# Performance work log

Hardware: AMD Instinct MI355X
Metric: run time of the kernel (lower is better)

Reference implementation:

```python
import jax, jax.numpy as jnp
import numpy as np

V, E, EH, H = 32000, 512, 1024, 512  # vocab, emb_dim, enc_hidden, dec_hidden
B, S = 16, 128


def setup_inputs() -> dict:
    key = jax.random.key(0)
    ks = jax.random.split(key, 8)
    g = lambda k, shape, scale: (jax.random.normal(k, shape, jnp.float32) * scale)
    return {
        "y": jax.random.randint(ks[0], (B, S), 0, V),
        "hn": jax.random.normal(ks[1], (B, 1, EH), jnp.float32),
        "emb": g(ks[2], (V, E), 0.02),          # embedding table
        "W_ih": g(ks[3], (3 * H, E), 0.05),      # GRU input weights (r,z,n)
        "W_hh": g(ks[4], (3 * H, H), 0.05),      # GRU hidden weights (r,z,n)
        "b_ih": jnp.zeros((3 * H,), jnp.float32),
        "b_hh": jnp.zeros((3 * H,), jnp.float32),
        "fc_w": g(ks[5], (H, EH), 0.03),         # fc: enc_hidden -> dec_hidden
        "fc_b": jnp.zeros((H,), jnp.float32),
        "pred_w": g(ks[6], (V, H), 0.03),        # pred: dec_hidden -> vocab
        "pred_b": jnp.zeros((V,), jnp.float32),
    }


def gru_scan(x, h0, W_ih, W_hh, b_ih, b_hh):
    """Single-layer unidirectional GRU (PyTorch gate order r,z,n).
    x: [B,S,E], h0: [B,H] -> outputs [B,S,H]."""
    h_dim = h0.shape[-1]
    # precompute input projections for all timesteps: [B,S,3H]
    gx = jnp.einsum('bse,ge->bsg', x, W_ih) + b_ih
    Wr, Wz, Wn = W_hh[:h_dim], W_hh[h_dim:2 * h_dim], W_hh[2 * h_dim:]
    br, bz, bn = b_hh[:h_dim], b_hh[h_dim:2 * h_dim], b_hh[2 * h_dim:]

    def step(h, g):
        gr, gz, gn = g[:, :h_dim], g[:, h_dim:2 * h_dim], g[:, 2 * h_dim:]
        r = jax.nn.sigmoid(gr + h @ Wr.T + br)
        z = jax.nn.sigmoid(gz + h @ Wz.T + bz)
        n = jnp.tanh(gn + r * (h @ Wn.T + bn))
        h_new = (1.0 - z) * n + z * h
        return h_new, h_new

    _, outs = jax.lax.scan(step, h0, jnp.swapaxes(gx, 0, 1))  # [S,B,H]
    return jnp.swapaxes(outs, 0, 1)  # [B,S,H]


def reference(y, hn, emb, W_ih, W_hh, b_ih, b_hh, fc_w, fc_b, pred_w, pred_b):
    # hn: [B,1,EH] -> fc -> [B,1,H] -> permute(1,0,2) -> initial hidden [B,H]
    h0 = (hn @ fc_w.T + fc_b)[:, 0, :]
    x = emb[y]  # [B,S,E]; dropout is identity in eval mode
    out = gru_scan(x, h0, W_ih, W_hh, b_ih, b_hh)  # [B,S,H]
    return out @ pred_w.T + pred_b  # [B,S,V]
```

## Files before the change

### kernel.cpp

```cpp
#include <hip/hip_runtime.h>


typedef __attribute__((ext_vector_type(8))) short           bf8_t;
typedef __attribute__((ext_vector_type(8))) unsigned short  us8_t;
typedef __attribute__((ext_vector_type(4))) unsigned short  us4_t;
typedef __attribute__((ext_vector_type(4))) float           f4_t;
typedef __attribute__((ext_vector_type(4))) unsigned int    u4_t;

#define SENT 0xFFFFFFFFu

__device__ __forceinline__ unsigned short f2bf(float x) {
    unsigned u = __builtin_bit_cast(unsigned, x);
    u += 0x7FFFu + ((u >> 16) & 1u);
    return (unsigned short)(u >> 16);
}
__device__ __forceinline__ float sigm(float x) { return 1.0f / (1.0f + __expf(-x)); }

__device__ __forceinline__ bf8_t mk_frag(f4_t v0, f4_t v1) {
    bf8_t f;
    f[0] = (short)f2bf(v0[0]); f[1] = (short)f2bf(v0[1]);
    f[2] = (short)f2bf(v0[2]); f[3] = (short)f2bf(v0[3]);
    f[4] = (short)f2bf(v1[0]); f[5] = (short)f2bf(v1[1]);
    f[6] = (short)f2bf(v1[2]); f[7] = (short)f2bf(v1[3]);
    return f;
}

__device__ __forceinline__ void llc_store_u32(unsigned int* p, unsigned int v) {
    asm volatile("global_store_dword %0, %1, off sc0 sc1" :: "v"(p), "v"(v) : "memory");
}

__global__ void k_fill(unsigned int* __restrict__ p) {
    int i = blockIdx.x * blockDim.x + threadIdx.x;
    u4_t v = {SENT, SENT, SENT, SENT};
    ((u4_t*)p)[i] = v;
}

__global__ void k_conv(const float* __restrict__ src, unsigned short* __restrict__ dst, int n4) {
    int i = blockIdx.x * blockDim.x + threadIdx.x;
    int stride = gridDim.x * blockDim.x;
    for (; i < n4; i += stride) {
        f4_t v = ((const f4_t*)src)[i];
        us4_t o;
        o[0] = f2bf(v[0]); o[1] = f2bf(v[1]); o[2] = f2bf(v[2]); o[3] = f2bf(v[3]);
        ((us4_t*)dst)[i] = o;
    }
}

__global__ void k_gather(const int* __restrict__ y, const float* __restrict__ emb,
                         unsigned short* __restrict__ xbf) {
    int m = blockIdx.x;
    int row = y[m];
    int t = threadIdx.x;
    f4_t v = ((const f4_t*)(emb + (size_t)row * 512))[t];
    us4_t o;
    o[0] = f2bf(v[0]); o[1] = f2bf(v[1]); o[2] = f2bf(v[2]); o[3] = f2bf(v[3]);
    ((us4_t*)(xbf + (size_t)m * 512))[t] = o;
}

__global__ void k_h0(const float* __restrict__ hn, const float* __restrict__ fc_w,
                     const float* __restrict__ fc_b, float* __restrict__ h0m) {
    __shared__ float sh[1024];
    int b = blockIdx.x, t = threadIdx.x;
    for (int i = t; i < 1024; i += 256) sh[i] = hn[b * 1024 + i];
    __syncthreads();
    int j = t;
    float a0 = fc_b[j], a1 = fc_b[j + 256];
    const float* w0 = fc_w + (size_t)j * 1024;
    const float* w1 = fc_w + (size_t)(j + 256) * 1024;
    #pragma unroll 8
    for (int e = 0; e < 1024; e++) { float he = sh[e]; a0 += he * w0[e]; a1 += he * w1[e]; }
    h0m[b * 512 + j] = a0;
    h0m[b * 512 + j + 256] = a1;
}

__launch_bounds__(256)
__global__ void k_gemm(const unsigned short* __restrict__ A, const unsigned short* __restrict__ Bt,
                       const float* __restrict__ bias, float* __restrict__ C, int N) {
    __shared__ unsigned short sA[128 * 64];
    __shared__ unsigned short sB[128 * 64];
    const int m0 = blockIdx.y * 128, n0 = blockIdx.x * 128;
    const int tid = threadIdx.x, lane = tid & 63, wave = tid >> 6;
    const int wm = wave >> 1, wn = wave & 1;
    f4_t acc[4][4] = {};
    for (int ks = 0; ks < 8; ks++) {
        const int k0 = ks * 64;
        #pragma unroll
        for (int t = 0; t < 4; t++) {
            int idx = tid + t * 256;
            int row = idx >> 3, slot = idx & 7;
            int sw = ((slot ^ (row & 7)) << 3);
            *(us8_t*)(&sA[row * 64 + sw]) = *(const us8_t*)(A + (size_t)(m0 + row) * 512 + k0 + slot * 8);
            *(us8_t*)(&sB[row * 64 + sw]) = *(const us8_t*)(Bt + (size_t)(n0 + row) * 512 + k0 + slot * 8);
        }
        __syncthreads();
        #pragma unroll
        for (int kk = 0; kk < 2; kk++) {
            bf8_t af[4], bfr[4];
            #pragma unroll
            for (int mi = 0; mi < 4; mi++) {
                int row = wm * 64 + mi * 16 + (lane & 15);
                int slot = (kk * 4 + (lane >> 4)) ^ (row & 7);
                af[mi] = *(const bf8_t*)(&sA[row * 64 + slot * 8]);
            }
            #pragma unroll
            for (int ni = 0; ni < 4; ni++) {
                int row = wn * 64 + ni * 16 + (lane & 15);
                int slot = (kk * 4 + (lane >> 4)) ^ (row & 7);
                bfr[ni] = *(const bf8_t*)(&sB[row * 64 + slot * 8]);
            }
            #pragma unroll
            for (int mi = 0; mi < 4; mi++)
                #pragma unroll
                for (int ni = 0; ni < 4; ni++)
                    acc[mi][ni] = __builtin_amdgcn_mfma_f32_16x16x32_bf16(af[mi], bfr[ni], acc[mi][ni], 0, 0, 0);
        }
        __syncthreads();
    }
    #pragma unroll
    for (int ni = 0; ni < 4; ni++) {
        int col = n0 + wn * 64 + ni * 16 + (lane & 15);
        float bv = bias[col];
        #pragma unroll
        for (int mi = 0; mi < 4; mi++) {
            int rbase = m0 + wm * 64 + mi * 16 + (lane >> 4) * 4;
            #pragma unroll
            for (int r = 0; r < 4; r++)
                C[(size_t)(rbase + r) * N + col] = acc[mi][ni][r] + bv;
        }
    }
}

__launch_bounds__(128, 1)
__global__ void k_rec(const float* __restrict__ W_hh, const float* __restrict__ b_hh,
                      const float* __restrict__ gx, const float* __restrict__ h0m,
                      unsigned int* __restrict__ hbuf, unsigned short* __restrict__ Hout) {
    const int c = blockIdx.x;
    const int tid = threadIdx.x;
    const int lane = tid & 63;
    const int w = tid >> 6;
    const int col = c * 16 + (lane & 15);
    const int kgrp = lane >> 4;
    const int bbase = kgrp * 4;

    __shared__ float sPart[2][12][64];

    bf8_t wfR[8], wfZ[8], wfN[8];
    {
        const f4_t* wr = (const f4_t*)(W_hh + (size_t)col * 512);
        const f4_t* wz = (const f4_t*)(W_hh + (size_t)(512 + col) * 512);
        const f4_t* wn = (const f4_t*)(W_hh + (size_t)(1024 + col) * 512);
        const int fo = kgrp * 2;
        #pragma unroll
        for (int j = 0; j < 8; j++) {
            const int kk = w * 8 + j;
            wfR[j] = mk_frag(wr[kk * 8 + fo], wr[kk * 8 + fo + 1]);
            wfZ[j] = mk_frag(wz[kk * 8 + fo], wz[kk * 8 + fo + 1]);
            wfN[j] = mk_frag(wn[kk * 8 + fo], wn[kk * 8 + fo + 1]);
        }
    }

    float brv = 0.f, bzv = 0.f, bnv = 0.f;
    f4_t h_reg = {0.f, 0.f, 0.f, 0.f};
    if (w == 0) {
        brv = b_hh[col]; bzv = b_hh[512 + col]; bnv = b_hh[1024 + col];
        #pragma unroll
        for (int r = 0; r < 4; r++) h_reg[r] = h0m[(bbase + r) * 512 + col];
        #pragma unroll
        for (int r = 0; r < 4; r++) {
            unsigned int hb = f2bf(h_reg[r]);
            unsigned int pr = __shfl_xor(hb, 1, 64);
            if (!(lane & 1))
                llc_store_u32(&hbuf[(bbase + r) * 256 + (col >> 1)], hb | (pr << 16));
        }
    }

    for (int s = 1; s <= 128; s++) {
        float gxr[4], gxz[4], gxn[4];
        if (w == 0) {
            #pragma unroll
            for (int r = 0; r < 4; r++) {
                const float* gp = gx + (size_t)((bbase + r) * 128 + (s - 1)) * 1536 + col;
                gxr[r] = gp[0]; gxz[r] = gp[512]; gxn[r] = gp[1024];
            }
        }

        const unsigned int* base = hbuf + (size_t)(s - 1) * 4096
                                 + (lane & 15) * 256 + kgrp * 4 + w * 128;
        u4_t q[8];
        int spins = 0;
        bool ok;
        do {
            asm volatile(
                "global_load_dwordx4 %0, %8, off sc0 sc1\n\t"
                "global_load_dwordx4 %1, %8, off offset:64 sc0 sc1\n\t"
                "global_load_dwordx4 %2, %8, off offset:128 sc0 sc1\n\t"
                "global_load_dwordx4 %3, %8, off offset:192 sc0 sc1\n\t"
                "global_load_dwordx4 %4, %8, off offset:256 sc0 sc1\n\t"
                "global_load_dwordx4 %5, %8, off offset:320 sc0 sc1\n\t"
                "global_load_dwordx4 %6, %8, off offset:384 sc0 sc1\n\t"
                "global_load_dwordx4 %7, %8, off offset:448 sc0 sc1\n\t"
                "s_waitcnt vmcnt(0)"
                : "=&v"(q[0]), "=&v"(q[1]), "=&v"(q[2]), "=&v"(q[3]),
                  "=&v"(q[4]), "=&v"(q[5]), "=&v"(q[6]), "=&v"(q[7])
                : "v"(base)
                : "memory");
            ok = true;
            #pragma unroll
            for (int j = 0; j < 8; j++)
                #pragma unroll
                for (int i = 0; i < 4; i++)
                    ok = ok && (q[j][i] != SENT);
        } while (!__all(ok) && ++spins < (1 << 20));
        __builtin_amdgcn_sched_barrier(0);

        f4_t aR = {}, aZ = {}, aN = {};
        #pragma unroll
        for (int j = 0; j < 8; j++) {
            bf8_t af = __builtin_bit_cast(bf8_t, q[j]);
            aR = __builtin_amdgcn_mfma_f32_16x16x32_bf16(af, wfR[j], aR, 0, 0, 0);
            aZ = __builtin_amdgcn_mfma_f32_16x16x32_bf16(af, wfZ[j], aZ, 0, 0, 0);
            aN = __builtin_amdgcn_mfma_f32_16x16x32_bf16(af, wfN[j], aN, 0, 0, 0);
        }

        const int slot = s & 1;
        if (w == 1) {
            #pragma unroll
            for (int r = 0; r < 4; r++) {
                sPart[slot][r][lane]     = aR[r];
                sPart[slot][4 + r][lane] = aZ[r];
                sPart[slot][8 + r][lane] = aN[r];
            }
        }
        __syncthreads();
        if (w == 0) {
            #pragma unroll
            for (int r = 0; r < 4; r++) {
                const int b = bbase + r;
                float pR = aR[r] + sPart[slot][r][lane];
                float pZ = aZ[r] + sPart[slot][4 + r][lane];
                float pN = aN[r] + sPart[slot][8 + r][lane];
                float rr = sigm(gxr[r] + pR + brv);
                float zz = sigm(gxz[r] + pZ + bzv);
                float nn = tanhf(gxn[r] + rr * (pN + bnv));
                float hnew = (1.f - zz) * nn + zz * h_reg[r];
                h_reg[r] = hnew;
                unsigned int hb = f2bf(hnew);
                Hout[(size_t)(b * 128 + (s - 1)) * 512 + col] = (unsigned short)hb;
                unsigned int pr = __shfl_xor(hb, 1, 64);
                if (!(lane & 1))
                    llc_store_u32(&hbuf[(size_t)s * 4096 + b * 256 + (col >> 1)], hb | (pr << 16));
            }
        }
    }
}

extern "C" void kernel_launch(void* const* d_in, const int* in_sizes, int n_in,
                              void* d_out, int out_size, void* d_ws, size_t ws_size,
                              hipStream_t stream) {
    const int*   y      = (const int*)  d_in[0];
    const float* hn     = (const float*)d_in[1];
    const float* emb    = (const float*)d_in[2];
    const float* W_ih   = (const float*)d_in[3];
    const float* W_hh   = (const float*)d_in[4];
    const float* b_ih   = (const float*)d_in[5];
    const float* b_hh   = (const float*)d_in[6];
    const float* fc_w   = (const float*)d_in[7];
    const float* fc_b   = (const float*)d_in[8];
    const float* pred_w = (const float*)d_in[9];
    const float* pred_b = (const float*)d_in[10];
    float* out = (float*)d_out;

    char* ws = (char*)d_ws;
    size_t off = 0;
    auto alloc = [&](size_t bytes) { void* p = ws + off; off = (off + bytes + 255) & ~(size_t)255; return p; };
    unsigned int*   hbuf   = (unsigned int*)   alloc((size_t)129 * 4096 * 4);
    float*          h0m    = (float*)          alloc((size_t)16 * 512 * 4);
    float*          gx     = (float*)          alloc((size_t)2048 * 1536 * 4);
    unsigned short* Hout   = (unsigned short*) alloc((size_t)2048 * 512 * 2);
    unsigned short* xbf    = (unsigned short*) alloc((size_t)2048 * 512 * 2);
    unsigned short* wihbf  = (unsigned short*) alloc((size_t)1536 * 512 * 2);
    unsigned short* pwbf   = (unsigned short*) alloc((size_t)32000 * 512 * 2);
    (void)ws_size; (void)in_sizes; (void)n_in; (void)out_size;

    k_fill  <<<516,  256, 0, stream>>>(hbuf);
    k_conv  <<<4096, 256, 0, stream>>>(pred_w, pwbf, 32000 * 512 / 4);
    k_conv  <<<512,  256, 0, stream>>>(W_ih,  wihbf, 1536 * 512 / 4);
    k_gather<<<2048, 128, 0, stream>>>(y, emb, xbf);
    k_h0    <<<16,   256, 0, stream>>>(hn, fc_w, fc_b, h0m);
    dim3 gG(12, 16);
    k_gemm  <<<gG, 256, 0, stream>>>(xbf, wihbf, b_ih, gx, 1536);
    k_rec   <<<32, 128, 0, stream>>>(W_hh, b_hh, gx, h0m, hbuf, Hout);
    dim3 gP(250, 16);
    k_gemm  <<<gP, 256, 0, stream>>>(Hout, pwbf, pred_b, out, 32000);
}
```

Before: 692.4 us.

## Fuse GRU recurrence with vocab projection GEMM via persistent tile queue

Merges the recurrent kernel and the output projection GEMM into one persistent kernel of 256 blocks. Sixteen blocks run the GRU scan with 32 columns each, and the remaining blocks pull output tiles from an atomic ticket. Each tile waits on sentinel-marked hidden states, so the projection overlaps with later timesteps. Hidden states are stored in timestep-major order and the output index is permuted back. Sigmoid and tanh are replaced with rcp/exp approximations. The change risks spinning blocks competing for resources and lower accuracy in the activations.

Result: faster. 645.0 us (-6.8%).

```diff
diff --git a/kernel.cpp b/kernel.cpp
--- a/kernel.cpp
+++ b/kernel.cpp
@@ -14,7 +14,13 @@
     u += 0x7FFFu + ((u >> 16) & 1u);
     return (unsigned short)(u >> 16);
 }
-__device__ __forceinline__ float sigm(float x) { return 1.0f / (1.0f + __expf(-x)); }
+__device__ __forceinline__ float fsigm(float x) {
+    return __builtin_amdgcn_rcpf(1.f + __expf(-x));
+}
+__device__ __forceinline__ float ftanh(float x) {
+    float e = __expf(2.f * x);
+    return 1.f - 2.f * __builtin_amdgcn_rcpf(e + 1.f);
+}
 
 __device__ __forceinline__ bf8_t mk_frag(f4_t v0, f4_t v1) {
     bf8_t f;
@@ -29,10 +35,13 @@
     asm volatile("global_store_dword %0, %1, off sc0 sc1" :: "v"(p), "v"(v) : "memory");
 }
 
-__global__ void k_fill(unsigned int* __restrict__ p) {
+__global__ void k_fill(unsigned int* __restrict__ hbuf, unsigned int* __restrict__ hout,
+                       int* __restrict__ ticket) {
+    if (blockIdx.x == 0 && threadIdx.x == 0) *ticket = 0;
     int i = blockIdx.x * blockDim.x + threadIdx.x;
     u4_t v = {SENT, SENT, SENT, SENT};
-    ((u4_t*)p)[i] = v;
+    if (i < 132096) ((u4_t*)hbuf)[i] = v;
+    else            ((u4_t*)hout)[i - 132096] = v;
 }
 
 __global__ void k_conv(const float* __restrict__ src, unsigned short* __restrict__ dst, int n4) {
@@ -130,125 +139,252 @@
     }
 }
 
-__launch_bounds__(128, 1)
-__global__ void k_rec(const float* __restrict__ W_hh, const float* __restrict__ b_hh,
-                      const float* __restrict__ gx, const float* __restrict__ h0m,
-                      unsigned int* __restrict__ hbuf, unsigned short* __restrict__ Hout) {
-    const int c = blockIdx.x;
+__launch_bounds__(256, 1)
+__global__ void k_fused(const float* __restrict__ W_hh, const float* __restrict__ b_hh,
+                        const float* __restrict__ gx, const float* __restrict__ h0m,
+                        unsigned int* __restrict__ hbuf, unsigned int* __restrict__ HoutP,
+                        const unsigned short* __restrict__ pwbf, const float* __restrict__ pred_b,
+                        float* __restrict__ out, int* __restrict__ tticket) {
+    __shared__ __align__(16) unsigned char smem[32768];
+    __shared__ int s_tile;
     const int tid = threadIdx.x;
     const int lane = tid & 63;
-    const int w = tid >> 6;
-    const int col = c * 16 + (lane & 15);
-    const int kgrp = lane >> 4;
-    const int bbase = kgrp * 4;
-
-    __shared__ float sPart[2][12][64];
-
-    bf8_t wfR[8], wfZ[8], wfN[8];
-    {
-        const f4_t* wr = (const f4_t*)(W_hh + (size_t)col * 512);
-        const f4_t* wz = (const f4_t*)(W_hh + (size_t)(512 + col) * 512);
-        const f4_t* wn = (const f4_t*)(W_hh + (size_t)(1024 + col) * 512);
-        const int fo = kgrp * 2;
-        #pragma unroll
-        for (int j = 0; j < 8; j++) {
-            const int kk = w * 8 + j;
-            wfR[j] = mk_frag(wr[kk * 8 + fo], wr[kk * 8 + fo + 1]);
-            wfZ[j] = mk_frag(wz[kk * 8 + fo], wz[kk * 8 + fo + 1]);
-            wfN[j] = mk_frag(wn[kk * 8 + fo], wn[kk * 8 + fo + 1]);
-        }
-    }
-
-    float brv = 0.f, bzv = 0.f, bnv = 0.f;
-    f4_t h_reg = {0.f, 0.f, 0.f, 0.f};
-    if (w == 0) {
-        brv = b_hh[col]; bzv = b_hh[512 + col]; bnv = b_hh[1024 + col];
-        #pragma unroll
-        for (int r = 0; r < 4; r++) h_reg[r] = h0m[(bbase + r) * 512 + col];
-        #pragma unroll
-        for (int r = 0; r < 4; r++) {
-            unsigned int hb = f2bf(h_reg[r]);
-            unsigned int pr = __shfl_xor(hb, 1, 64);
-            if (!(lane & 1))
-                llc_store_u32(&hbuf[(bbase + r) * 256 + (col >> 1)], hb | (pr << 16));
-        }
-    }
-
-    for (int s = 1; s <= 128; s++) {
-        float gxr[4], gxz[4], gxn[4];
+    const int wave = tid >> 6;
+
+    if (blockIdx.x < 16) {
+        float* sPart = (float*)smem;
+        const int c = blockIdx.x;
+        const int ch = wave >> 1, w = wave & 1;
+        const int col = c * 32 + ch * 16 + (lane & 15);
+        const int kgrp = lane >> 4, bbase = kgrp * 4;
+
+        bf8_t wfR[8], wfZ[8], wfN[8];
+        {
+            const f4_t* wr = (const f4_t*)(W_hh + (size_t)col * 512);
+            const f4_t* wz = (const f4_t*)(W_hh + (size_t)(512 + col) * 512);
+            const f4_t* wn = (const f4_t*)(W_hh + (size_t)(1024 + col) * 512);
+            const int fo = kgrp * 2;
+            #pragma unroll
+            for (int j = 0; j < 8; j++) {
+                const int kk = w * 8 + j;
+                wfR[j] = mk_frag(wr[kk * 8 + fo], wr[kk * 8 + fo + 1]);
+                wfZ[j] = mk_frag(wz[kk * 8 + fo], wz[kk * 8 + fo + 1]);
+                wfN[j] = mk_frag(wn[kk * 8 + fo], wn[kk * 8 + fo + 1]);
+            }
+        }
+        float brv = 0.f, bzv = 0.f, bnv = 0.f;
+        f4_t h_reg = {0.f, 0.f, 0.f, 0.f};
         if (w == 0) {
+            brv = b_hh[col]; bzv = b_hh[512 + col]; bnv = b_hh[1024 + col];
+            #pragma unroll
+            for (int r = 0; r < 4; r++) h_reg[r] = h0m[(bbase + r) * 512 + col];
             #pragma unroll
             for (int r = 0; r < 4; r++) {
-                const float* gp = gx + (size_t)((bbase + r) * 128 + (s - 1)) * 1536 + col;
-                gxr[r] = gp[0]; gxz[r] = gp[512]; gxn[r] = gp[1024];
-            }
-        }
-
-        const unsigned int* base = hbuf + (size_t)(s - 1) * 4096
-                                 + (lane & 15) * 256 + kgrp * 4 + w * 128;
-        u4_t q[8];
-        int spins = 0;
-        bool ok;
-        do {
-            asm volatile(
-                "global_load_dwordx4 %0, %8, off sc0 sc1\n\t"
-                "global_load_dwordx4 %1, %8, off offset:64 sc0 sc1\n\t"
-                "global_load_dwordx4 %2, %8, off offset:128 sc0 sc1\n\t"
-                "global_load_dwordx4 %3, %8, off offset:192 sc0 sc1\n\t"
-                "global_load_dwordx4 %4, %8, off offset:256 sc0 sc1\n\t"
-                "global_load_dwordx4 %5, %8, off offset:320 sc0 sc1\n\t"
-                "global_load_dwordx4 %6, %8, off offset:384 sc0 sc1\n\t"
-                "global_load_dwordx4 %7, %8, off offset:448 sc0 sc1\n\t"
-                "s_waitcnt vmcnt(0)"
-                : "=&v"(q[0]), "=&v"(q[1]), "=&v"(q[2]), "=&v"(q[3]),
-                  "=&v"(q[4]), "=&v"(q[5]), "=&v"(q[6]), "=&v"(q[7])
-                : "v"(base)
-                : "memory");
-            ok = true;
-            #pragma unroll
-            for (int j = 0; j < 8; j++)
-                #pragma unroll
-                for (int i = 0; i < 4; i++)
-                    ok = ok && (q[j][i] != SENT);
-        } while (!__all(ok) && ++spins < (1 << 20));
-        __builtin_amdgcn_sched_barrier(0);
-
-        f4_t aR = {}, aZ = {}, aN = {};
-        #pragma unroll
-        for (int j = 0; j < 8; j++) {
-            bf8_t af = __builtin_bit_cast(bf8_t, q[j]);
-            aR = __builtin_amdgcn_mfma_f32_16x16x32_bf16(af, wfR[j], aR, 0, 0, 0);
-            aZ = __builtin_amdgcn_mfma_f32_16x16x32_bf16(af, wfZ[j], aZ, 0, 0, 0);
-            aN = __builtin_amdgcn_mfma_f32_16x16x32_bf16(af, wfN[j], aN, 0, 0, 0);
-        }
-
-        const int slot = s & 1;
-        if (w == 1) {
-            #pragma unroll
-            for (int r = 0; r < 4; r++) {
-                sPart[slot][r][lane]     = aR[r];
-                sPart[slot][4 + r][lane] = aZ[r];
-                sPart[slot][8 + r][lane] = aN[r];
-            }
-        }
-        __syncthreads();
-        if (w == 0) {
-            #pragma unroll
-            for (int r = 0; r < 4; r++) {
-                const int b = bbase + r;
-                float pR = aR[r] + sPart[slot][r][lane];
-                float pZ = aZ[r] + sPart[slot][4 + r][lane];
-                float pN = aN[r] + sPart[slot][8 + r][lane];
-                float rr = sigm(gxr[r] + pR + brv);
-                float zz = sigm(gxz[r] + pZ + bzv);
-                float nn = tanhf(gxn[r] + rr * (pN + bnv));
-                float hnew = (1.f - zz) * nn + zz * h_reg[r];
-                h_reg[r] = hnew;
-                unsigned int hb = f2bf(hnew);
-                Hout[(size_t)(b * 128 + (s - 1)) * 512 + col] = (unsigned short)hb;
+                unsigned int hb = f2bf(h_reg[r]);
                 unsigned int pr = __shfl_xor(hb, 1, 64);
                 if (!(lane & 1))
-                    llc_store_u32(&hbuf[(size_t)s * 4096 + b * 256 + (col >> 1)], hb | (pr << 16));
+                    llc_store_u32(&hbuf[(bbase + r) * 256 + (col >> 1)], hb | (pr << 16));
+            }
+        }
+
+        for (int s = 1; s <= 128; s++) {
+            float gxr[4], gxz[4], gxn[4];
+            if (w == 0) {
+                #pragma unroll
+                for (int r = 0; r < 4; r++) {
+                    const float* gp = gx + (size_t)((bbase + r) * 128 + (s - 1)) * 1536 + col;
+                    gxr[r] = gp[0]; gxz[r] = gp[512]; gxn[r] = gp[1024];
+                }
+            }
+            const unsigned int* base = hbuf + (size_t)(s - 1) * 4096
+                                     + (lane & 15) * 256 + kgrp * 4 + w * 128;
+            u4_t q[8];
+            int spins = 0;
+            bool ok;
+            do {
+                asm volatile(
+                    "global_load_dwordx4 %0, %8, off sc0 sc1\n\t"
+                    "global_load_dwordx4 %1, %8, off offset:64 sc0 sc1\n\t"
+                    "global_load_dwordx4 %2, %8, off offset:128 sc0 sc1\n\t"
+                    "global_load_dwordx4 %3, %8, off offset:192 sc0 sc1\n\t"
+                    "global_load_dwordx4 %4, %8, off offset:256 sc0 sc1\n\t"
+                    "global_load_dwordx4 %5, %8, off offset:320 sc0 sc1\n\t"
+                    "global_load_dwordx4 %6, %8, off offset:384 sc0 sc1\n\t"
+                    "global_load_dwordx4 %7, %8, off offset:448 sc0 sc1\n\t"
+                    "s_waitcnt vmcnt(0)"
+                    : "=&v"(q[0]), "=&v"(q[1]), "=&v"(q[2]), "=&v"(q[3]),
+                      "=&v"(q[4]), "=&v"(q[5]), "=&v"(q[6]), "=&v"(q[7])
+                    : "v"(base)
+                    : "memory");
+                ok = true;
+                #pragma unroll
+                for (int j = 0; j < 8; j++)
+                    #pragma unroll
+                    for (int i = 0; i < 4; i++)
+                        ok = ok && (q[j][i] != SENT);
+            } while (!__all(ok) && ++spins < (1 << 20));
+            __builtin_amdgcn_sched_barrier(0);
+
+            f4_t aR = {}, aZ = {}, aN = {};
+            #pragma unroll
+            for (int j = 0; j < 8; j++) {
+                bf8_t af = __builtin_bit_cast(bf8_t, q[j]);
+                aR = __builtin_amdgcn_mfma_f32_16x16x32_bf16(af, wfR[j], aR, 0, 0, 0);
+                aZ = __builtin_amdgcn_mfma_f32_16x16x32_bf16(af, wfZ[j], aZ, 0, 0, 0);
+                aN = __builtin_amdgcn_mfma_f32_16x16x32_bf16(af, wfN[j], aN, 0, 0, 0);
+            }
+
+            const int slot = s & 1;
+            if (w == 1) {
+                #pragma unroll
+                for (int r = 0; r < 4; r++) {
+                    sPart[((slot * 2 + ch) * 12 + r) * 64 + lane]     = aR[r];
+                    sPart[((slot * 2 + ch) * 12 + 4 + r) * 64 + lane] = aZ[r];
+                    sPart[((slot * 2 + ch) * 12 + 8 + r) * 64 + lane] = aN[r];
+                }
+            }
+            __syncthreads();
+            if (w == 0) {
+                unsigned int hb[4];
+                #pragma unroll
+                for (int r = 0; r < 4; r++) {
+                    float pR = aR[r] + sPart[((slot * 2 + ch) * 12 + r) * 64 + lane];
+                    float pZ = aZ[r] + sPart[((slot * 2 + ch) * 12 + 4 + r) * 64 + lane];
+                    float pN = aN[r] + sPart[((slot * 2 + ch) * 12 + 8 + r) * 64 + lane];
+                    float rr = fsigm(gxr[r] + pR + brv);
+                    float zz = fsigm(gxz[r] + pZ + bzv);
+                    float nn = ftanh(gxn[r] + rr * (pN + bnv));
+                    float hnew = (1.f - zz) * nn + zz * h_reg[r];
+                    h_reg[r] = hnew;
+                    hb[r] = f2bf(hnew);
+                }
+                #pragma unroll
+                for (int r = 0; r < 4; r++) {
+                    unsigned int pr = __shfl_xor(hb[r], 1, 64);
+                    if (!(lane & 1))
+                        llc_store_u32(&hbuf[(size_t)s * 4096 + (bbase + r) * 256 + (col >> 1)],
+                                      hb[r] | (pr << 16));
+                }
+                #pragma unroll
+                for (int r = 0; r < 4; r++) {
+                    unsigned int pr = __shfl_xor(hb[r], 1, 64);
+                    if (!(lane & 1))
+                        llc_store_u32(&HoutP[(size_t)((s - 1) * 16 + bbase + r) * 256 + (col >> 1)],
+                                      hb[r] | (pr << 16));
+                }
+            }
+        }
+        __syncthreads();
+    }
+
+    unsigned short* sA = (unsigned short*)smem;
+    unsigned short* sB = sA + 8192;
+    const int wm = wave >> 1, wn = wave & 1;
+    const unsigned short* A = (const unsigned short*)HoutP;
+
+    int rowA[4], slotA[4];
+    #pragma unroll
+    for (int t4 = 0; t4 < 4; t4++) {
+        int idx = tid + t4 * 256;
+        rowA[t4] = idx >> 3; slotA[t4] = idx & 7;
+    }
+
+    for (;;) {
+        if (tid == 0) s_tile = atomicAdd(tticket, 1);
+        __syncthreads();
+        const int t = s_tile;
+        __syncthreads();
+        if (t >= 4000) break;
+        const int tm = t / 250, tn = t - tm * 250;
+        const int m0 = tm * 128, n0 = tn * 128;
+
+        if (tid == 0) {
+            const unsigned int* probe = HoutP + (size_t)(m0 + 127) * 256 + 255;
+            unsigned v; int guard = 0;
+            do {
+                asm volatile("global_load_dword %0, %1, off sc0 sc1\n\ts_waitcnt vmcnt(0)"
+                             : "=&v"(v) : "v"(probe) : "memory");
+                if (v == SENT) __builtin_amdgcn_s_sleep(16);
+            } while (v == SENT && ++guard < (1 << 20));
+        }
+        __syncthreads();
+
+        f4_t acc[4][4] = {};
+        for (int ks = 0; ks < 8; ks++) {
+            const int k0 = ks * 64;
+            #pragma unroll
+            for (int t4 = 0; t4 < 4; t4++) {
+                int row = rowA[t4], slot = slotA[t4];
+                int sw = ((slot ^ (row & 7)) << 3);
+                *(us8_t*)(&sB[row * 64 + sw]) =
+                    *(const us8_t*)(pwbf + (size_t)(n0 + row) * 512 + k0 + slot * 8);
+            }
+            {
+                const unsigned short* p0 = A + (size_t)(m0 + rowA[0]) * 512 + k0 + slotA[0] * 8;
+                const unsigned short* p1 = A + (size_t)(m0 + rowA[1]) * 512 + k0 + slotA[1] * 8;
+                const unsigned short* p2 = A + (size_t)(m0 + rowA[2]) * 512 + k0 + slotA[2] * 8;
+                const unsigned short* p3 = A + (size_t)(m0 + rowA[3]) * 512 + k0 + slotA[3] * 8;
+                u4_t a0, a1, a2, a3;
+                int spins = 0; bool okk;
+                do {
+                    asm volatile(
+                        "global_load_dwordx4 %0, %4, off sc0 sc1\n\t"
+                        "global_load_dwordx4 %1, %5, off sc0 sc1\n\t"
+                        "global_load_dwordx4 %2, %6, off sc0 sc1\n\t"
+                        "global_load_dwordx4 %3, %7, off sc0 sc1\n\t"
+                        "s_waitcnt vmcnt(0)"
+                        : "=&v"(a0), "=&v"(a1), "=&v"(a2), "=&v"(a3)
+                        : "v"(p0), "v"(p1), "v"(p2), "v"(p3)
+                        : "memory");
+                    okk = true;
+                    #pragma unroll
+                    for (int i = 0; i < 4; i++)
+                        okk = okk && (a0[i] != SENT) && (a1[i] != SENT)
+                                  && (a2[i] != SENT) && (a3[i] != SENT);
+                    if (!okk) __builtin_amdgcn_s_sleep(1);
+                } while (!okk && ++spins < (1 << 20));
+                __builtin_amdgcn_sched_barrier(0);
+                *(u4_t*)(&sA[rowA[0] * 64 + ((slotA[0] ^ (rowA[0] & 7)) << 3)]) = a0;
+                *(u4_t*)(&sA[rowA[1] * 64 + ((slotA[1] ^ (rowA[1] & 7)) << 3)]) = a1;
+                *(u4_t*)(&sA[rowA[2] * 64 + ((slotA[2] ^ (rowA[2] & 7)) << 3)]) = a2;
+                *(u4_t*)(&sA[rowA[3] * 64 + ((slotA[3] ^ (rowA[3] & 7)) << 3)]) = a3;
+            }
+            __syncthreads();
+            #pragma unroll
+            for (int kk = 0; kk < 2; kk++) {
+                bf8_t af[4], bfr[4];
+                #pragma unroll
+                for (int mi = 0; mi < 4; mi++) {
+                    int row = wm * 64 + mi * 16 + (lane & 15);
+                    int slot = (kk * 4 + (lane >> 4)) ^ (row & 7);
+                    af[mi] = *(const bf8_t*)(&sA[row * 64 + slot * 8]);
+                }
+                #pragma unroll
+                for (int ni = 0; ni < 4; ni++) {
+                    int row = wn * 64 + ni * 16 + (lane & 15);
+                    int slot = (kk * 4 + (lane >> 4)) ^ (row & 7);
+                    bfr[ni] = *(const bf8_t*)(&sB[row * 64 + slot * 8]);
+                }
+                #pragma unroll
+                for (int mi = 0; mi < 4; mi++)
+                    #pragma unroll
+                    for (int ni = 0; ni < 4; ni++)
+                        acc[mi][ni] = __builtin_amdgcn_mfma_f32_16x16x32_bf16(af[mi], bfr[ni], acc[mi][ni], 0, 0, 0);
+            }
+            __syncthreads();
+        }
+        #pragma unroll
+        for (int ni = 0; ni < 4; ni++) {
+            int colI = n0 + wn * 64 + ni * 16 + (lane & 15);
+            float bv = pred_b[colI];
+            #pragma unroll
+            for (int mi = 0; mi < 4; mi++) {
+                int rbase = m0 + wm * 64 + mi * 16 + (lane >> 4) * 4;
+                #pragma unroll
+                for (int r = 0; r < 4; r++) {
+                    int mr = rbase + r;
+                    out[(size_t)((mr & 15) * 128 + (mr >> 4)) * 32000 + colI] = acc[mi][ni][r] + bv;
+                }
             }
         }
     }
@@ -274,22 +410,22 @@
     size_t off = 0;
     auto alloc = [&](size_t bytes) { void* p = ws + off; off = (off + bytes + 255) & ~(size_t)255; return p; };
     unsigned int*   hbuf   = (unsigned int*)   alloc((size_t)129 * 4096 * 4);
+    unsigned int*   HoutP  = (unsigned int*)   alloc((size_t)2048 * 256 * 4);
+    int*            tticket= (int*)            alloc(256);
     float*          h0m    = (float*)          alloc((size_t)16 * 512 * 4);
     float*          gx     = (float*)          alloc((size_t)2048 * 1536 * 4);
-    unsigned short* Hout   = (unsigned short*) alloc((size_t)2048 * 512 * 2);
     unsigned short* xbf    = (unsigned short*) alloc((size_t)2048 * 512 * 2);
     unsigned short* wihbf  = (unsigned short*) alloc((size_t)1536 * 512 * 2);
     unsigned short* pwbf   = (unsigned short*) alloc((size_t)32000 * 512 * 2);
     (void)ws_size; (void)in_sizes; (void)n_in; (void)out_size;
 
-    k_fill  <<<516,  256, 0, stream>>>(hbuf);
+    k_fill  <<<1028, 256, 0, stream>>>(hbuf, HoutP, tticket);
     k_conv  <<<4096, 256, 0, stream>>>(pred_w, pwbf, 32000 * 512 / 4);
     k_conv  <<<512,  256, 0, stream>>>(W_ih,  wihbf, 1536 * 512 / 4);
     k_gather<<<2048, 128, 0, stream>>>(y, emb, xbf);
     k_h0    <<<16,   256, 0, stream>>>(hn, fc_w, fc_b, h0m);
     dim3 gG(12, 16);
     k_gemm  <<<gG, 256, 0, stream>>>(xbf, wihbf, b_ih, gx, 1536);
-    k_rec   <<<32, 128, 0, stream>>>(W_hh, b_hh, gx, h0m, hbuf, Hout);
-    dim3 gP(250, 16);
-    k_gemm  <<<gP, 256, 0, stream>>>(Hout, pwbf, pred_b, out, 32000);
-}
+    k_fused <<<256, 256, 0, stream>>>(W_hh, b_hh, gx, h0m, hbuf, HoutP,
+                                      pwbf, pred_b, out, tticket);
+}
```
